# Kernel optimization log

Measured on AMD Instinct MI355X. Metric: run time of the kernel, lower is better.

Reference implementation:

```python
import jax, jax.numpy as jnp
import numpy as np

J = 1.0
B, C, L = 16, 16, 128


def _masks(L):
    ii, jj = jnp.meshgrid(jnp.arange(L), jnp.arange(L), indexing='ij')
    black = ((ii + jj) % 2 == 0)
    return black, jnp.logical_not(black)


def _nbr_sum(s):
    # periodic up/down/left/right neighbor sum, same math as the (i±1)%L gathers
    return (jnp.roll(s, 1, -2) + jnp.roll(s, -1, -2)
            + jnp.roll(s, 1, -1) + jnp.roll(s, -1, -1))


def _half_update(spins, mask, T, key):
    # Metropolis on one checkerboard color: dE = 2*J*s*sum_nbrs
    dE = 2.0 * J * spins * _nbr_sum(spins)
    u = jax.random.uniform(key, spins.shape, dtype=spins.dtype)
    accept = u < jnp.exp(-dE / T[:, None, None, None])
    return jnp.where(jnp.logical_and(accept, mask), -spins, spins)


def _one_sweep(spins, T, key, black, white):
    k1, k2 = jax.random.split(key)
    spins = _half_update(spins, black, T, k1)
    return _half_update(spins, white, T, k2)


def _energy(spins):
    # E = -J * sum over bonds (right + down neighbors once each) -> [B, C]
    return -J * jnp.sum(spins * (jnp.roll(spins, -1, -2) + jnp.roll(spins, -1, -1)), axis=(-2, -1))


def _pt_exchange(spins, T, key):
    nB = T.shape[0]
    P = nB // 2
    E = _energy(spins)                       # [B, C]
    beta = 1.0 / T
    E0, E1 = E[0:2 * P:2], E[1:2 * P:2]
    d = (beta[0:2 * P:2] - beta[1:2 * P:2])[:, None] * (E0 - E1)  # [P, C]
    u = jax.random.uniform(key, d.shape, dtype=spins.dtype)
    # accept prob min(1, exp(d)); exp(min(d,0)) is overflow-safe and equivalent
    acc = (u < jnp.exp(jnp.minimum(d, 0.0)))[:, :, None, None]
    s0, s1 = spins[0:2 * P:2], spins[1:2 * P:2]
    spins = spins.at[0:2 * P:2].set(jnp.where(acc, s1, s0))
    spins = spins.at[1:2 * P:2].set(jnp.where(acc, s0, s1))
    return spins


def _simulate(spins_init, T, n_sweeps, n_therm, decorrelate, pt_interval):
    Lx = spins_init.shape[-1]
    black, white = _masks(Lx)
    base = jax.random.key(42)

    def step_fn(spins, i):
        k = jax.random.fold_in(base, i)
        spins = _one_sweep(spins, T, k, black, white)
        spins = jax.lax.cond(i % pt_interval == 0,
                             lambda s: _pt_exchange(s, T, jax.random.fold_in(k, 123)),
                             lambda s: s, spins)
        return spins, None

    # thermalization
    spins, _ = jax.lax.scan(step_fn, spins_init, jnp.arange(n_therm))

    # production: record one sample per decorrelate sweeps
    num_samples = n_sweeps // decorrelate

    def block_fn(spins, b):
        spins, _ = jax.lax.scan(lambda s, j: step_fn(s, n_therm + b * decorrelate + j),
                                spins, jnp.arange(decorrelate))
        return spins, spins

    spins, samples = jax.lax.scan(block_fn, spins, jnp.arange(num_samples))
    # samples: [S, B, C, L, L] -> [B, C*S, L, L]
    Bn, Cn = spins.shape[0], spins.shape[1]
    return jnp.transpose(samples, (1, 0, 2, 3, 4)).reshape(Bn, num_samples * Cn, Lx, Lx)


def setup_inputs() -> dict:
    key = jax.random.key(0)
    k1, _ = jax.random.split(key)
    x = jax.random.normal(k1, (B, C, L, L), dtype=jnp.float32)
    spins_init = jnp.where(x >= 0, 1.0, -1.0).astype(jnp.float32)  # ±1 Ising spins
    T = jnp.linspace(1.0, 3.5, B).astype(jnp.float32)              # temperature ladder
    return {"spins_init": spins_init, "T": T, "n_sweeps": 10, "n_therm": 10,
            "decorrelate": 5, "pt_interval": 5}


def reference(spins_init, T, n_sweeps, n_therm, decorrelate, pt_interval):
    return _simulate(spins_init, T, n_sweeps, n_therm, decorrelate, pt_interval)
```

## Files before the change

### kernel.cpp

```cpp
#include <hip/hip_runtime.h>
#include <stdint.h>


#define LSZ   128
#define NB    16
#define NC    16
#define NSITES (NB*NC*LSZ*LSZ)

__host__ __device__ __forceinline__ void tf2x32(uint32_t k0, uint32_t k1,
                                                uint32_t x0, uint32_t x1,
                                                uint32_t& o0, uint32_t& o1) {
  uint32_t k2 = k0 ^ k1 ^ 0x1BD11BDAu;
  x0 += k0; x1 += k1;
#define TFR(r) { x0 += x1; x1 = (x1 << (r)) | (x1 >> (32 - (r))); x1 ^= x0; }
  TFR(13) TFR(15) TFR(26) TFR(6)
  x0 += k1; x1 += k2 + 1u;
  TFR(17) TFR(29) TFR(16) TFR(24)
  x0 += k2; x1 += k0 + 2u;
  TFR(13) TFR(15) TFR(26) TFR(6)
  x0 += k0; x1 += k1 + 3u;
  TFR(17) TFR(29) TFR(16) TFR(24)
  x0 += k1; x1 += k2 + 4u;
  TFR(13) TFR(15) TFR(26) TFR(6)
  x0 += k2; x1 += k0 + 5u;
#undef TFR
  o0 = x0; o1 = x1;
}

__device__ __forceinline__ void tf2x32x2(uint32_t k0, uint32_t k1,
                                         uint32_t xa, uint32_t xb,
                                         uint32_t& oa, uint32_t& ob) {
  uint32_t k2 = k0 ^ k1 ^ 0x1BD11BDAu;
  uint32_t a0 = k0, a1 = xa + k1;
  uint32_t b0 = k0, b1 = xb + k1;
#define TFR2(r) { a0 += a1; b0 += b1; \
                  a1 = __builtin_rotateleft32(a1, r); \
                  b1 = __builtin_rotateleft32(b1, r); \
                  a1 ^= a0; b1 ^= b0; }
  TFR2(13) TFR2(15) TFR2(26) TFR2(6)
  a0 += k1; a1 += k2 + 1u; b0 += k1; b1 += k2 + 1u;
  TFR2(17) TFR2(29) TFR2(16) TFR2(24)
  a0 += k2; a1 += k0 + 2u; b0 += k2; b1 += k0 + 2u;
  TFR2(13) TFR2(15) TFR2(26) TFR2(6)
  a0 += k0; a1 += k1 + 3u; b0 += k0; b1 += k1 + 3u;
  TFR2(17) TFR2(29) TFR2(16) TFR2(24)
  a0 += k1; a1 += k2 + 4u; b0 += k1; b1 += k2 + 4u;
  TFR2(13) TFR2(15) TFR2(26) TFR2(6)
  a0 += k2; a1 += k0 + 5u; b0 += k2; b1 += k0 + 5u;
#undef TFR2
  oa = a0 ^ a1;
  ob = b0 ^ b1;
}

__device__ __forceinline__ float tf_uniform(uint32_t w) {
  union { uint32_t u; float f; } cvt;
  cvt.u = (w >> 9) | 0x3f800000u;
  return cvt.f - 1.0f;
}

__device__ __forceinline__ int sb(uint32_t w, int b) {
  return (int)((int32_t)(w << ((3 - b) * 8)) >> 24);
}

__global__ __launch_bounds__(1024) void k_chunk(const float4* __restrict__ in4,
                                                uint32_t* __restrict__ sg,
                                                const float* __restrict__ T,
                                                int* __restrict__ slotmap,
                                                const float* __restrict__ Eprev,
                                                float* __restrict__ Ecur,
                                                float* __restrict__ out,
                                                int chunk, int start, int nsw,
                                                int sample_local, int sidx,
                                                int write_E, int store_back) {
  __shared__ __align__(16) uint32_t lat32[LSZ * LSZ / 4];
  __shared__ uint32_t kb[5][4];
  __shared__ uint32_t sh_T4, sh_T8;
  __shared__ int sh_bp;
  __shared__ int wred[16];

  const int w = blockIdx.x;
  const int t = threadIdx.x;
  const int c = w & 15;

  if (t < nsw) {
    uint32_t kk0, kk1, a, b;
    tf2x32(0u, 42u, 0u, (uint32_t)(start + t), kk0, kk1);
    tf2x32(kk0, kk1, 0u, 0u, a, b);
    kb[t][0] = a; kb[t][1] = b;
    tf2x32(kk0, kk1, 0u, 1u, a, b);
    kb[t][2] = a; kb[t][3] = b;
  }

  if (chunk == 0) {
    for (int k = 0; k < 4; ++k) {
      int idx = k * 1024 + t;
      float4 v = in4[(w << 12) + idx];
      lat32[idx] = (v.x >= 0.0f ? 0x01u : 0xFFu)
                 | ((v.y >= 0.0f ? 0x01u : 0xFFu) << 8)
                 | ((v.z >= 0.0f ? 0x01u : 0xFFu) << 16)
                 | ((v.w >= 0.0f ? 0x01u : 0xFFu) << 24);
    }
  } else {
    ((uint4*)lat32)[t] = ((const uint4*)sg)[(w << 10) + t];
  }

  if (t == 0) {
    int bp;
    if (chunk == 0) {
      bp = w >> 4;
    } else {
      bp = slotmap[w];
      int p = bp >> 1;
      float E0 = Eprev[(2 * p) * NC + c];
      float E1 = Eprev[(2 * p + 1) * NC + c];
      float b0 = 1.0f / T[2 * p];
      float b1 = 1.0f / T[2 * p + 1];
      float d = (b0 - b1) * (E0 - E1);
      uint32_t kk0, kk1, p0, p1, w0, w1;
      tf2x32(0u, 42u, 0u, (uint32_t)(start - 1), kk0, kk1);
      tf2x32(kk0, kk1, 0u, 123u, p0, p1);
      tf2x32(p0, p1, 0u, (uint32_t)(p * NC + c), w0, w1);
      float u = tf_uniform(w0 ^ w1);
      float pa = (d < 0.0f) ? (float)exp((double)d) : 1.0f;
      if (u < pa) bp ^= 1;
    }
    slotmap[w] = bp;
    sh_bp = bp;
    float Tb = T[bp];
    float p4 = (float)exp((double)(-4.0f / Tb));
    float p8 = (float)exp((double)(-8.0f / Tb));
    sh_T4 = (uint32_t)ceil((double)p4 * 8388608.0);
    sh_T8 = (uint32_t)ceil((double)p8 * 8388608.0);
  }
  __syncthreads();

  const int bp = sh_bp;
  const uint32_t T4 = sh_T4, T8 = sh_T8;
  const uint32_t TOPEN = 0x00800000u;
  const int r    = t >> 3;
  const int seg  = t & 7;
  const int col0 = seg << 4;
  const uint32_t rowbase = ((uint32_t)((bp << 4) | c) << 14) + ((uint32_t)r << 7);
  const int8_t* latb = (const int8_t*)lat32;
  const int own4 = (r << 3) + seg;

  for (int sw = 0; sw < nsw; ++sw) {
    for (int par = 0; par < 2; ++par) {
      const uint32_t kk0 = kb[sw][par * 2];
      const uint32_t kk1 = kb[sw][par * 2 + 1];
      const int j0 = (r + par) & 1;

      uint4 cv = ((const uint4*)lat32)[own4];
      uint4 uv = ((const uint4*)lat32)[(((r - 1) & 127) << 3) + seg];
      uint4 dv = ((const uint4*)lat32)[(((r + 1) & 127) << 3) + seg];
      int lfb = latb[(r << 7) + ((col0 - 1) & 127)];
      int rtb = latb[(r << 7) + ((col0 + 16) & 127)];

      uint32_t cw[4] = {cv.x, cv.y, cv.z, cv.w};
      uint32_t uw[4] = {uv.x, uv.y, uv.z, uv.w};
      uint32_t dw[4] = {dv.x, dv.y, dv.z, dv.w};

      uint32_t ext[5];
      ext[0] = (cw[0] << 8) | (uint32_t)(uint8_t)lfb;
      ext[1] = (cw[0] >> 24) | (cw[1] << 8);
      ext[2] = (cw[1] >> 24) | (cw[2] << 8);
      ext[3] = (cw[2] >> 24) | (cw[3] << 8);
      ext[4] = (cw[3] >> 24) | ((uint32_t)(uint8_t)rtb << 8);
      uint32_t Y[5], U[4], D[4];
#pragma unroll
      for (int i = 0; i < 4; ++i) {
        uint32_t sh = (ext[i] >> 8) | (ext[i + 1] << 24);
        Y[i] = j0 ? sh : ext[i];
        uint32_t su = (uw[i] >> 8) | ((i < 3 ? uw[i + 1] : 0u) << 24);
        U[i] = j0 ? su : uw[i];
        uint32_t sd = (dw[i] >> 8) | ((i < 3 ? dw[i + 1] : 0u) << 24);
        D[i] = j0 ? sd : dw[i];
      }
      Y[4] = j0 ? (ext[4] >> 8) : ext[4];

      const uint32_t mbase = 0xFEu << (8 * j0);
      uint32_t xm[4] = {0u, 0u, 0u, 0u};
      const uint32_t cnt0 = rowbase + (uint32_t)(col0 + j0);
#pragma unroll
      for (int m2 = 0; m2 < 4; ++m2) {
        const int ma = 2 * m2, mb = 2 * m2 + 1;
        int lfa = sb(Y[(2 * ma) >> 2], (2 * ma) & 3);
        int s0a = sb(Y[(2 * ma + 1) >> 2], (2 * ma + 1) & 3);
        int rta = sb(Y[(2 * ma + 2) >> 2], (2 * ma + 2) & 3);
        int upa = sb(U[(2 * ma) >> 2], (2 * ma) & 3);
        int dna = sb(D[(2 * ma) >> 2], (2 * ma) & 3);
        int qa = s0a * (lfa + rta + upa + dna);
        int lfb2 = sb(Y[(2 * mb) >> 2], (2 * mb) & 3);
        int s0b = sb(Y[(2 * mb + 1) >> 2], (2 * mb + 1) & 3);
        int rtb2 = sb(Y[(2 * mb + 2) >> 2], (2 * mb + 2) & 3);
        int upb = sb(U[(2 * mb) >> 2], (2 * mb) & 3);
        int dnb = sb(D[(2 * mb) >> 2], (2 * mb) & 3);
        int qb = s0b * (lfb2 + rtb2 + upb + dnb);
        uint32_t wa, wb;
        tf2x32x2(kk0, kk1, cnt0 + 2u * (uint32_t)ma, cnt0 + 2u * (uint32_t)mb,
                 wa, wb);
        uint32_t ta = (qa <= 0) ? TOPEN : (qa == 4 ? T8 : T4);
        uint32_t tb = (qb <= 0) ? TOPEN : (qb == 4 ? T8 : T4);
        if ((wa >> 9) < ta) xm[m2] |= mbase;
        if ((wb >> 9) < tb) xm[m2] |= (mbase << 16);
      }
      uint4 nv;
      nv.x = cw[0] ^ xm[0]; nv.y = cw[1] ^ xm[1];
      nv.z = cw[2] ^ xm[2]; nv.w = cw[3] ^ xm[3];
      ((uint4*)lat32)[own4] = nv;
      __syncthreads();
    }

    if (sw == sample_local) {
      uint4 cv = ((const uint4*)lat32)[own4];
      float4* dst = (float4*)out
                  + (((size_t)((bp << 5) + (sidx << 4) + c)) << 12)
                  + (r << 5) + (seg << 2);
      uint32_t wv[4] = {cv.x, cv.y, cv.z, cv.w};
#pragma unroll
      for (int qd = 0; qd < 4; ++qd) {
        float4 f;
        f.x = (float)sb(wv[qd], 0); f.y = (float)sb(wv[qd], 1);
        f.z = (float)sb(wv[qd], 2); f.w = (float)sb(wv[qd], 3);
        dst[qd] = f;
      }
    }
  }

  if (write_E) {
    uint4 cv = ((const uint4*)lat32)[own4];
    uint4 dv = ((const uint4*)lat32)[(((r + 1) & 127) << 3) + seg];
    int rb = latb[(r << 7) + ((col0 + 16) & 127)];
    uint32_t cw[4] = {cv.x, cv.y, cv.z, cv.w};
    uint32_t dw[4] = {dv.x, dv.y, dv.z, dv.w};
    int psum = 0;
#pragma unroll
    for (int i = 0; i < 16; ++i) {
      int ci = sb(cw[i >> 2], i & 3);
      int di = sb(dw[i >> 2], i & 3);
      int ri = (i < 15) ? sb(cw[(i + 1) >> 2], (i + 1) & 3) : rb;
      psum += ci * (di + ri);
    }
#pragma unroll
    for (int o = 32; o > 0; o >>= 1) psum += __shfl_down(psum, o, 64);
    if ((t & 63) == 0) wred[t >> 6] = psum;
    __syncthreads();
    if (t == 0) {
      int tot = 0;
#pragma unroll
      for (int i = 0; i < 16; ++i) tot += wred[i];
      Ecur[(bp << 4) | c] = -(float)tot;
    }
  }

  if (store_back) {
    ((uint4*)sg)[(w << 10) + t] = ((const uint4*)lat32)[t];
  }
}

extern "C" void kernel_launch(void* const* d_in, const int* in_sizes, int n_in,
                              void* d_out, int out_size, void* d_ws, size_t ws_size,
                              hipStream_t stream) {
  const float* spins_in = (const float*)d_in[0];
  const float* T        = (const float*)d_in[1];
  uint32_t* s   = (uint32_t*)d_ws;
  float*  Ea    = (float*)((char*)d_ws + (4u << 20));
  float*  Eb    = (float*)((char*)d_ws + (4u << 20) + 1024);
  int*  slotmap = (int*)((char*)d_ws + (4u << 20) + 2048);
  float*  out = (float*)d_out;

  const int starts[5]  = {0, 1, 6, 11, 16};
  const int counts[5]  = {1, 5, 5, 5, 4};
  const int samploc[5] = {-1, -1, -1, 3, 3};
  const int sampidx[5] = {0, 0, 0, 0, 1};
  const int writeE[5]  = {1, 1, 1, 1, 0};
  const int storeB[5]  = {1, 1, 1, 1, 0};

  for (int ch = 0; ch < 5; ++ch) {
    float* Ecur  = (ch & 1) ? Eb : Ea;
    float* Eprev = (ch & 1) ? Ea : Eb;
    k_chunk<<<256, 1024, 0, stream>>>((const float4*)spins_in, s, T, slotmap,
                                      Eprev, Ecur, out,
                                      ch, starts[ch], counts[ch],
                                      samploc[ch], sampidx[ch],
                                      writeE[ch], storeB[ch]);
  }
}
```

Measured before the change: 283.5 us.

## Update interior checkerboard rows per wave without a block barrier

Moves the per-site update into a helper, upd_seg. Each wavefront owns eight lattice rows, so after its black half-sweep it updates the white sites of its six interior rows straight away, separated only by a wave-level barrier. The white sites on each wave's two boundary rows are updated afterwards, by 256 threads, following a block-wide sync. The goal is to shorten the block-level synchronisation that separated the two half-sweeps. The cost is a third update phase that runs with only a quarter of the threads, and idle boundary-row lanes inside each wave during the interior update.

Result: slower. 302.9 us (+6.9%).

```diff
diff --git a/kernel.cpp b/kernel.cpp
--- a/kernel.cpp
+++ b/kernel.cpp
@@ -62,6 +62,75 @@
   return (int)((int32_t)(w << ((3 - b) * 8)) >> 24);
 }
 
+__device__ __forceinline__ void upd_seg(uint32_t* lat32, int r, int seg,
+                                        int j0, uint32_t kk0, uint32_t kk1,
+                                        uint32_t bpc14,
+                                        uint32_t T4, uint32_t T8) {
+  const uint32_t TOPEN = 0x00800000u;
+  const int8_t* latb = (const int8_t*)lat32;
+  const int col0 = seg << 4;
+  const int own4 = (r << 3) + seg;
+
+  uint4 cv = ((const uint4*)lat32)[own4];
+  uint4 uv = ((const uint4*)lat32)[(((r - 1) & 127) << 3) + seg];
+  uint4 dv = ((const uint4*)lat32)[(((r + 1) & 127) << 3) + seg];
+  int lfb = latb[(r << 7) + ((col0 - 1) & 127)];
+  int rtb = latb[(r << 7) + ((col0 + 16) & 127)];
+
+  uint32_t cw[4] = {cv.x, cv.y, cv.z, cv.w};
+  uint32_t uw[4] = {uv.x, uv.y, uv.z, uv.w};
+  uint32_t dw[4] = {dv.x, dv.y, dv.z, dv.w};
+
+  uint32_t ext[5];
+  ext[0] = (cw[0] << 8) | (uint32_t)(uint8_t)lfb;
+  ext[1] = (cw[0] >> 24) | (cw[1] << 8);
+  ext[2] = (cw[1] >> 24) | (cw[2] << 8);
+  ext[3] = (cw[2] >> 24) | (cw[3] << 8);
+  ext[4] = (cw[3] >> 24) | ((uint32_t)(uint8_t)rtb << 8);
+  uint32_t Y[5], U[4], D[4];
+#pragma unroll
+  for (int i = 0; i < 4; ++i) {
+    uint32_t sh = (ext[i] >> 8) | (ext[i + 1] << 24);
+    Y[i] = j0 ? sh : ext[i];
+    uint32_t su = (uw[i] >> 8) | ((i < 3 ? uw[i + 1] : 0u) << 24);
+    U[i] = j0 ? su : uw[i];
+    uint32_t sd = (dw[i] >> 8) | ((i < 3 ? dw[i + 1] : 0u) << 24);
+    D[i] = j0 ? sd : dw[i];
+  }
+  Y[4] = j0 ? (ext[4] >> 8) : ext[4];
+
+  const uint32_t mbase = 0xFEu << (8 * j0);
+  uint32_t xm[4] = {0u, 0u, 0u, 0u};
+  const uint32_t cnt0 = bpc14 + ((uint32_t)r << 7) + (uint32_t)(col0 + j0);
+#pragma unroll
+  for (int m2 = 0; m2 < 4; ++m2) {
+    const int ma = 2 * m2, mb = 2 * m2 + 1;
+    int lfa = sb(Y[(2 * ma) >> 2], (2 * ma) & 3);
+    int s0a = sb(Y[(2 * ma + 1) >> 2], (2 * ma + 1) & 3);
+    int rta = sb(Y[(2 * ma + 2) >> 2], (2 * ma + 2) & 3);
+    int upa = sb(U[(2 * ma) >> 2], (2 * ma) & 3);
+    int dna = sb(D[(2 * ma) >> 2], (2 * ma) & 3);
+    int qa = s0a * (lfa + rta + upa + dna);
+    int lfb2 = sb(Y[(2 * mb) >> 2], (2 * mb) & 3);
+    int s0b = sb(Y[(2 * mb + 1) >> 2], (2 * mb + 1) & 3);
+    int rtb2 = sb(Y[(2 * mb + 2) >> 2], (2 * mb + 2) & 3);
+    int upb = sb(U[(2 * mb) >> 2], (2 * mb) & 3);
+    int dnb = sb(D[(2 * mb) >> 2], (2 * mb) & 3);
+    int qb = s0b * (lfb2 + rtb2 + upb + dnb);
+    uint32_t wa, wb;
+    tf2x32x2(kk0, kk1, cnt0 + 2u * (uint32_t)ma, cnt0 + 2u * (uint32_t)mb,
+             wa, wb);
+    uint32_t ta = (qa <= 0) ? TOPEN : (qa == 4 ? T8 : T4);
+    uint32_t tb = (qb <= 0) ? TOPEN : (qb == 4 ? T8 : T4);
+    if ((wa >> 9) < ta) xm[m2] |= mbase;
+    if ((wb >> 9) < tb) xm[m2] |= (mbase << 16);
+  }
+  uint4 nv;
+  nv.x = cw[0] ^ xm[0]; nv.y = cw[1] ^ xm[1];
+  nv.z = cw[2] ^ xm[2]; nv.w = cw[3] ^ xm[3];
+  ((uint4*)lat32)[own4] = nv;
+}
+
 __global__ __launch_bounds__(1024) void k_chunk(const float4* __restrict__ in4,
                                                 uint32_t* __restrict__ sg,
                                                 const float* __restrict__ T,
@@ -136,83 +205,31 @@
 
   const int bp = sh_bp;
   const uint32_t T4 = sh_T4, T8 = sh_T8;
-  const uint32_t TOPEN = 0x00800000u;
-  const int r    = t >> 3;
-  const int seg  = t & 7;
-  const int col0 = seg << 4;
-  const uint32_t rowbase = ((uint32_t)((bp << 4) | c) << 14) + ((uint32_t)r << 7);
-  const int8_t* latb = (const int8_t*)lat32;
-  const int own4 = (r << 3) + seg;
+  const int r   = t >> 3;
+  const int seg = t & 7;
+  const uint32_t bpc14 = ((uint32_t)((bp << 4) | c) << 14);
+  const int rb8 = r & 7;
+  const bool interior = (rb8 != 0) && (rb8 != 7);
 
   for (int sw = 0; sw < nsw; ++sw) {
-    for (int par = 0; par < 2; ++par) {
-      const uint32_t kk0 = kb[sw][par * 2];
-      const uint32_t kk1 = kb[sw][par * 2 + 1];
-      const int j0 = (r + par) & 1;
-
-      uint4 cv = ((const uint4*)lat32)[own4];
-      uint4 uv = ((const uint4*)lat32)[(((r - 1) & 127) << 3) + seg];
-      uint4 dv = ((const uint4*)lat32)[(((r + 1) & 127) << 3) + seg];
-      int lfb = latb[(r << 7) + ((col0 - 1) & 127)];
-      int rtb = latb[(r << 7) + ((col0 + 16) & 127)];
-
-      uint32_t cw[4] = {cv.x, cv.y, cv.z, cv.w};
-      uint32_t uw[4] = {uv.x, uv.y, uv.z, uv.w};
-      uint32_t dw[4] = {dv.x, dv.y, dv.z, dv.w};
-
-      uint32_t ext[5];
-      ext[0] = (cw[0] << 8) | (uint32_t)(uint8_t)lfb;
-      ext[1] = (cw[0] >> 24) | (cw[1] << 8);
-      ext[2] = (cw[1] >> 24) | (cw[2] << 8);
-      ext[3] = (cw[2] >> 24) | (cw[3] << 8);
-      ext[4] = (cw[3] >> 24) | ((uint32_t)(uint8_t)rtb << 8);
-      uint32_t Y[5], U[4], D[4];
-#pragma unroll
-      for (int i = 0; i < 4; ++i) {
-        uint32_t sh = (ext[i] >> 8) | (ext[i + 1] << 24);
-        Y[i] = j0 ? sh : ext[i];
-        uint32_t su = (uw[i] >> 8) | ((i < 3 ? uw[i + 1] : 0u) << 24);
-        U[i] = j0 ? su : uw[i];
-        uint32_t sd = (dw[i] >> 8) | ((i < 3 ? dw[i + 1] : 0u) << 24);
-        D[i] = j0 ? sd : dw[i];
-      }
-      Y[4] = j0 ? (ext[4] >> 8) : ext[4];
-
-      const uint32_t mbase = 0xFEu << (8 * j0);
-      uint32_t xm[4] = {0u, 0u, 0u, 0u};
-      const uint32_t cnt0 = rowbase + (uint32_t)(col0 + j0);
-#pragma unroll
-      for (int m2 = 0; m2 < 4; ++m2) {
-        const int ma = 2 * m2, mb = 2 * m2 + 1;
-        int lfa = sb(Y[(2 * ma) >> 2], (2 * ma) & 3);
-        int s0a = sb(Y[(2 * ma + 1) >> 2], (2 * ma + 1) & 3);
-        int rta = sb(Y[(2 * ma + 2) >> 2], (2 * ma + 2) & 3);
-        int upa = sb(U[(2 * ma) >> 2], (2 * ma) & 3);
-        int dna = sb(D[(2 * ma) >> 2], (2 * ma) & 3);
-        int qa = s0a * (lfa + rta + upa + dna);
-        int lfb2 = sb(Y[(2 * mb) >> 2], (2 * mb) & 3);
-        int s0b = sb(Y[(2 * mb + 1) >> 2], (2 * mb + 1) & 3);
-        int rtb2 = sb(Y[(2 * mb + 2) >> 2], (2 * mb + 2) & 3);
-        int upb = sb(U[(2 * mb) >> 2], (2 * mb) & 3);
-        int dnb = sb(D[(2 * mb) >> 2], (2 * mb) & 3);
-        int qb = s0b * (lfb2 + rtb2 + upb + dnb);
-        uint32_t wa, wb;
-        tf2x32x2(kk0, kk1, cnt0 + 2u * (uint32_t)ma, cnt0 + 2u * (uint32_t)mb,
-                 wa, wb);
-        uint32_t ta = (qa <= 0) ? TOPEN : (qa == 4 ? T8 : T4);
-        uint32_t tb = (qb <= 0) ? TOPEN : (qb == 4 ? T8 : T4);
-        if ((wa >> 9) < ta) xm[m2] |= mbase;
-        if ((wb >> 9) < tb) xm[m2] |= (mbase << 16);
-      }
-      uint4 nv;
-      nv.x = cw[0] ^ xm[0]; nv.y = cw[1] ^ xm[1];
-      nv.z = cw[2] ^ xm[2]; nv.w = cw[3] ^ xm[3];
-      ((uint4*)lat32)[own4] = nv;
-      __syncthreads();
-    }
+    const uint32_t bk0 = kb[sw][0], bk1 = kb[sw][1];
+    const uint32_t wk0 = kb[sw][2], wk1 = kb[sw][3];
+
+    upd_seg(lat32, r, seg, r & 1, bk0, bk1, bpc14, T4, T8);
+    __builtin_amdgcn_wave_barrier();
+    if (interior)
+      upd_seg(lat32, r, seg, (r + 1) & 1, wk0, wk1, bpc14, T4, T8);
+    __syncthreads();
+
+    if (t < 256) {
+      int idx = t >> 3;
+      int er  = ((idx >> 1) << 3) + ((idx & 1) ? 7 : 0);
+      upd_seg(lat32, er, t & 7, (er + 1) & 1, wk0, wk1, bpc14, T4, T8);
+    }
+    __syncthreads();
 
     if (sw == sample_local) {
-      uint4 cv = ((const uint4*)lat32)[own4];
+      uint4 cv = ((const uint4*)lat32)[(r << 3) + seg];
       float4* dst = (float4*)out
                   + (((size_t)((bp << 5) + (sidx << 4) + c)) << 12)
                   + (r << 5) + (seg << 2);
@@ -228,7 +245,9 @@
   }
 
   if (write_E) {
-    uint4 cv = ((const uint4*)lat32)[own4];
+    const int8_t* latb = (const int8_t*)lat32;
+    const int col0 = seg << 4;
+    uint4 cv = ((const uint4*)lat32)[(r << 3) + seg];
     uint4 dv = ((const uint4*)lat32)[(((r + 1) & 127) << 3) + seg];
     int rb = latb[(r << 7) + ((col0 + 16) & 127)];
     uint32_t cw[4] = {cv.x, cv.y, cv.z, cv.w};
```

## Store lattice as checkerboard-split 0/1 bytes with SWAR neighbor counts and LUT thresholds

Applied to the files above, without the earlier changes.

Spins are re-encoded as 0/1 bytes and each row is split by column parity into two half-planes. The four neighbor spins can then be summed with packed byte adds, and the acceptance threshold comes from a 16-entry shared LUT indexed by spin and neighbor count. This replaces the per-site sign-extension arithmetic. Energy is computed with XOR bond counts and a byte popcount via multiply. The aim is fewer ALU ops per site around the RNG, at the cost of extra shared memory lookups and the sign-bit unpacking when writing output.

New measurement: 267.6 us. 1.06x faster.

```diff
diff --git a/kernel.cpp b/kernel.cpp
--- a/kernel.cpp
+++ b/kernel.cpp
@@ -58,10 +58,6 @@
   return cvt.f - 1.0f;
 }
 
-__device__ __forceinline__ int sb(uint32_t w, int b) {
-  return (int)((int32_t)(w << ((3 - b) * 8)) >> 24);
-}
-
 __global__ __launch_bounds__(1024) void k_chunk(const float4* __restrict__ in4,
                                                 uint32_t* __restrict__ sg,
                                                 const float* __restrict__ T,
@@ -74,13 +70,15 @@
                                                 int write_E, int store_back) {
   __shared__ __align__(16) uint32_t lat32[LSZ * LSZ / 4];
   __shared__ uint32_t kb[5][4];
-  __shared__ uint32_t sh_T4, sh_T8;
+  __shared__ uint32_t sh_lut[16];
   __shared__ int sh_bp;
   __shared__ int wred[16];
 
   const int w = blockIdx.x;
   const int t = threadIdx.x;
   const int c = w & 15;
+  const int r = t >> 3;
+  const int h = t & 7;
 
   if (t < nsw) {
     uint32_t kk0, kk1, a, b;
@@ -92,14 +90,23 @@
   }
 
   if (chunk == 0) {
+    uint32_t pw[2][2] = {{0u, 0u}, {0u, 0u}};
+#pragma unroll
     for (int k = 0; k < 4; ++k) {
-      int idx = k * 1024 + t;
-      float4 v = in4[(w << 12) + idx];
-      lat32[idx] = (v.x >= 0.0f ? 0x01u : 0xFFu)
-                 | ((v.y >= 0.0f ? 0x01u : 0xFFu) << 8)
-                 | ((v.z >= 0.0f ? 0x01u : 0xFFu) << 16)
-                 | ((v.w >= 0.0f ? 0x01u : 0xFFu) << 24);
-    }
+      float4 v = in4[(w << 12) + (r << 5) + (h << 2) + k];
+      uint32_t b0 = v.x >= 0.0f ? 1u : 0u;
+      uint32_t b1 = v.y >= 0.0f ? 1u : 0u;
+      uint32_t b2 = v.z >= 0.0f ? 1u : 0u;
+      uint32_t b3 = v.w >= 0.0f ? 1u : 0u;
+      int word = k >> 1, sh = (k & 1) * 16;
+      pw[0][word] |= (b0 | (b2 << 8)) << sh;
+      pw[1][word] |= (b1 | (b3 << 8)) << sh;
+    }
+    int base = (r << 4) + (h << 1);
+    lat32[base]          = pw[0][0];
+    lat32[base + 1]      = pw[0][1];
+    lat32[2048 + base]     = pw[1][0];
+    lat32[2048 + base + 1] = pw[1][1];
   } else {
     ((uint4*)lat32)[t] = ((const uint4*)sg)[(w << 10) + t];
   }
@@ -129,118 +136,110 @@
     float Tb = T[bp];
     float p4 = (float)exp((double)(-4.0f / Tb));
     float p8 = (float)exp((double)(-8.0f / Tb));
-    sh_T4 = (uint32_t)ceil((double)p4 * 8388608.0);
-    sh_T8 = (uint32_t)ceil((double)p8 * 8388608.0);
+    uint32_t T4 = (uint32_t)ceil((double)p4 * 8388608.0);
+    uint32_t T8 = (uint32_t)ceil((double)p8 * 8388608.0);
+    const uint32_t TOPEN = 0x00800000u;
+    for (int i = 0; i < 16; ++i) {
+      int ob = i >> 3, n = i & 7;
+      uint32_t th = TOPEN;
+      if (ob) { if (n == 3) th = T4; else if (n == 4) th = T8; }
+      else    { if (n == 1) th = T4; else if (n == 0) th = T8; }
+      sh_lut[i] = th;
+    }
   }
   __syncthreads();
 
   const int bp = sh_bp;
-  const uint32_t T4 = sh_T4, T8 = sh_T8;
-  const uint32_t TOPEN = 0x00800000u;
-  const int r    = t >> 3;
-  const int seg  = t & 7;
-  const int col0 = seg << 4;
-  const uint32_t rowbase = ((uint32_t)((bp << 4) | c) << 14) + ((uint32_t)r << 7);
-  const int8_t* latb = (const int8_t*)lat32;
-  const int own4 = (r << 3) + seg;
+  const uint32_t bpc14 = ((uint32_t)((bp << 4) | c) << 14);
+  const uint8_t* latb = (const uint8_t*)lat32;
 
   for (int sw = 0; sw < nsw; ++sw) {
     for (int par = 0; par < 2; ++par) {
       const uint32_t kk0 = kb[sw][par * 2];
       const uint32_t kk1 = kb[sw][par * 2 + 1];
-      const int j0 = (r + par) & 1;
-
-      uint4 cv = ((const uint4*)lat32)[own4];
-      uint4 uv = ((const uint4*)lat32)[(((r - 1) & 127) << 3) + seg];
-      uint4 dv = ((const uint4*)lat32)[(((r + 1) & 127) << 3) + seg];
-      int lfb = latb[(r << 7) + ((col0 - 1) & 127)];
-      int rtb = latb[(r << 7) + ((col0 + 16) & 127)];
-
-      uint32_t cw[4] = {cv.x, cv.y, cv.z, cv.w};
-      uint32_t uw[4] = {uv.x, uv.y, uv.z, uv.w};
-      uint32_t dw[4] = {dv.x, dv.y, dv.z, dv.w};
-
-      uint32_t ext[5];
-      ext[0] = (cw[0] << 8) | (uint32_t)(uint8_t)lfb;
-      ext[1] = (cw[0] >> 24) | (cw[1] << 8);
-      ext[2] = (cw[1] >> 24) | (cw[2] << 8);
-      ext[3] = (cw[2] >> 24) | (cw[3] << 8);
-      ext[4] = (cw[3] >> 24) | ((uint32_t)(uint8_t)rtb << 8);
-      uint32_t Y[5], U[4], D[4];
-#pragma unroll
-      for (int i = 0; i < 4; ++i) {
-        uint32_t sh = (ext[i] >> 8) | (ext[i + 1] << 24);
-        Y[i] = j0 ? sh : ext[i];
-        uint32_t su = (uw[i] >> 8) | ((i < 3 ? uw[i + 1] : 0u) << 24);
-        U[i] = j0 ? su : uw[i];
-        uint32_t sd = (dw[i] >> 8) | ((i < 3 ? dw[i + 1] : 0u) << 24);
-        D[i] = j0 ? sd : dw[i];
+      const int tp = (r + par) & 1;
+      const int sp = tp ^ 1;
+
+      const int ob = (tp << 11) + (r << 4) + (h << 1);
+      const int ub = (tp << 11) + (((r - 1) & 127) << 4) + (h << 1);
+      const int db = (tp << 11) + (((r + 1) & 127) << 4) + (h << 1);
+      const int sb = (sp << 11) + (r << 4) + (h << 1);
+
+      uint2 O = *(const uint2*)(lat32 + ob);
+      uint2 U = *(const uint2*)(lat32 + ub);
+      uint2 D = *(const uint2*)(lat32 + db);
+      uint2 S = *(const uint2*)(lat32 + sb);
+      const int ei = tp ? (((h << 3) + 8) & 63) : (((h << 3) - 1) & 63);
+      uint32_t e = latb[(sp << 13) + (r << 6) + ei];
+
+      uint32_t s0e = (S.x << 8) | e;
+      uint32_t s1e = (S.y << 8) | (S.x >> 24);
+      uint32_t s0o = (S.x >> 8) | (S.y << 24);
+      uint32_t s1o = (S.y >> 8) | (e << 24);
+      uint32_t sh0 = tp ? s0o : s0e;
+      uint32_t sh1 = tp ? s1o : s1e;
+
+      uint32_t n0 = U.x + D.x + S.x + sh0;
+      uint32_t n1 = U.y + D.y + S.y + sh1;
+      uint32_t i0 = (O.x << 3) | n0;
+      uint32_t i1 = (O.y << 3) | n1;
+
+      uint32_t fb = 0;
+      const uint32_t cnt0 = bpc14 + ((uint32_t)r << 7) + (uint32_t)((h << 4) + tp);
+#pragma unroll
+      for (int m2 = 0; m2 < 4; ++m2) {
+        const int ma = 2 * m2, mb2 = 2 * m2 + 1;
+        uint32_t iwa = (ma < 4) ? i0 : i1;
+        uint32_t iwb = (mb2 < 4) ? i0 : i1;
+        uint32_t tha = sh_lut[(iwa >> (8 * (ma & 3))) & 15];
+        uint32_t thb = sh_lut[(iwb >> (8 * (mb2 & 3))) & 15];
+        uint32_t wa, wb;
+        tf2x32x2(kk0, kk1, cnt0 + 2u * (uint32_t)ma, cnt0 + 2u * (uint32_t)mb2,
+                 wa, wb);
+        fb |= ((wa >> 9) < tha) ? (1u << ma) : 0u;
+        fb |= ((wb >> 9) < thb) ? (1u << mb2) : 0u;
       }
-      Y[4] = j0 ? (ext[4] >> 8) : ext[4];
-
-      const uint32_t mbase = 0xFEu << (8 * j0);
-      uint32_t xm[4] = {0u, 0u, 0u, 0u};
-      const uint32_t cnt0 = rowbase + (uint32_t)(col0 + j0);
-#pragma unroll
-      for (int m2 = 0; m2 < 4; ++m2) {
-        const int ma = 2 * m2, mb = 2 * m2 + 1;
-        int lfa = sb(Y[(2 * ma) >> 2], (2 * ma) & 3);
-        int s0a = sb(Y[(2 * ma + 1) >> 2], (2 * ma + 1) & 3);
-        int rta = sb(Y[(2 * ma + 2) >> 2], (2 * ma + 2) & 3);
-        int upa = sb(U[(2 * ma) >> 2], (2 * ma) & 3);
-        int dna = sb(D[(2 * ma) >> 2], (2 * ma) & 3);
-        int qa = s0a * (lfa + rta + upa + dna);
-        int lfb2 = sb(Y[(2 * mb) >> 2], (2 * mb) & 3);
-        int s0b = sb(Y[(2 * mb + 1) >> 2], (2 * mb + 1) & 3);
-        int rtb2 = sb(Y[(2 * mb + 2) >> 2], (2 * mb + 2) & 3);
-        int upb = sb(U[(2 * mb) >> 2], (2 * mb) & 3);
-        int dnb = sb(D[(2 * mb) >> 2], (2 * mb) & 3);
-        int qb = s0b * (lfb2 + rtb2 + upb + dnb);
-        uint32_t wa, wb;
-        tf2x32x2(kk0, kk1, cnt0 + 2u * (uint32_t)ma, cnt0 + 2u * (uint32_t)mb,
-                 wa, wb);
-        uint32_t ta = (qa <= 0) ? TOPEN : (qa == 4 ? T8 : T4);
-        uint32_t tb = (qb <= 0) ? TOPEN : (qb == 4 ? T8 : T4);
-        if ((wa >> 9) < ta) xm[m2] |= mbase;
-        if ((wb >> 9) < tb) xm[m2] |= (mbase << 16);
-      }
-      uint4 nv;
-      nv.x = cw[0] ^ xm[0]; nv.y = cw[1] ^ xm[1];
-      nv.z = cw[2] ^ xm[2]; nv.w = cw[3] ^ xm[3];
-      ((uint4*)lat32)[own4] = nv;
+      uint32_t xm0 = (fb & 1u) | ((fb & 2u) << 7) | ((fb & 4u) << 14)
+                   | ((fb & 8u) << 21);
+      uint32_t xm1 = ((fb >> 4) & 1u) | ((fb & 32u) << 3) | ((fb & 64u) << 10)
+                   | ((fb & 128u) << 17);
+      lat32[ob]     = O.x ^ xm0;
+      lat32[ob + 1] = O.y ^ xm1;
       __syncthreads();
     }
 
     if (sw == sample_local) {
-      uint4 cv = ((const uint4*)lat32)[own4];
+      uint2 A = *(const uint2*)(lat32 + (r << 4) + (h << 1));
+      uint2 B = *(const uint2*)(lat32 + 2048 + (r << 4) + (h << 1));
       float4* dst = (float4*)out
                   + (((size_t)((bp << 5) + (sidx << 4) + c)) << 12)
-                  + (r << 5) + (seg << 2);
-      uint32_t wv[4] = {cv.x, cv.y, cv.z, cv.w};
+                  + (r << 5) + (h << 2);
+      uint32_t aw[2] = {A.x, A.y}, bw[2] = {B.x, B.y};
 #pragma unroll
       for (int qd = 0; qd < 4; ++qd) {
+        int lb = 2 * qd;
         float4 f;
-        f.x = (float)sb(wv[qd], 0); f.y = (float)sb(wv[qd], 1);
-        f.z = (float)sb(wv[qd], 2); f.w = (float)sb(wv[qd], 3);
+        f.x = ((aw[lb >> 2] >> (8 * (lb & 3))) & 1u) ? 1.0f : -1.0f;
+        f.y = ((bw[lb >> 2] >> (8 * (lb & 3))) & 1u) ? 1.0f : -1.0f;
+        int lb1 = lb + 1;
+        f.z = ((aw[lb1 >> 2] >> (8 * (lb1 & 3))) & 1u) ? 1.0f : -1.0f;
+        f.w = ((bw[lb1 >> 2] >> (8 * (lb1 & 3))) & 1u) ? 1.0f : -1.0f;
         dst[qd] = f;
       }
     }
   }
 
   if (write_E) {
-    uint4 cv = ((const uint4*)lat32)[own4];
-    uint4 dv = ((const uint4*)lat32)[(((r + 1) & 127) << 3) + seg];
-    int rb = latb[(r << 7) + ((col0 + 16) & 127)];
-    uint32_t cw[4] = {cv.x, cv.y, cv.z, cv.w};
-    uint32_t dw[4] = {dv.x, dv.y, dv.z, dv.w};
-    int psum = 0;
-#pragma unroll
-    for (int i = 0; i < 16; ++i) {
-      int ci = sb(cw[i >> 2], i & 3);
-      int di = sb(dw[i >> 2], i & 3);
-      int ri = (i < 15) ? sb(cw[(i + 1) >> 2], (i + 1) & 3) : rb;
-      psum += ci * (di + ri);
-    }
+    uint2 A0 = *(const uint2*)(lat32 + (r << 4) + (h << 1));
+    uint2 A1 = *(const uint2*)(lat32 + 2048 + (r << 4) + (h << 1));
+    uint2 D0 = *(const uint2*)(lat32 + (((r + 1) & 127) << 4) + (h << 1));
+    uint2 D1 = *(const uint2*)(lat32 + 2048 + (((r + 1) & 127) << 4) + (h << 1));
+    uint32_t e2 = latb[(r << 6) + (((h << 3) + 8) & 63)];
+    uint32_t xs0 = (A0.x >> 8) | (A0.y << 24);
+    uint32_t xs1 = (A0.y >> 8) | (e2 << 24);
+    uint32_t tx = (A0.x ^ D0.x) + (A1.x ^ D1.x) + (A0.x ^ A1.x) + (A1.x ^ xs0);
+    uint32_t ty = (A0.y ^ D0.y) + (A1.y ^ D1.y) + (A0.y ^ A1.y) + (A1.y ^ xs1);
+    int psum = (int)((tx * 0x01010101u) >> 24) + (int)((ty * 0x01010101u) >> 24);
 #pragma unroll
     for (int o = 32; o > 0; o >>= 1) psum += __shfl_down(psum, o, 64);
     if ((t & 63) == 0) wred[t >> 6] = psum;
@@ -249,7 +248,7 @@
       int tot = 0;
 #pragma unroll
       for (int i = 0; i < 16; ++i) tot += wred[i];
-      Ecur[(bp << 4) | c] = -(float)tot;
+      Ecur[(bp << 4) | c] = (float)(2 * tot - 32768);
     }
   }
 
```
